# Performance work log

Hardware: AMD Instinct MI355X
Metric: run time of the kernel (lower is better)

Reference implementation:

```python
import jax, jax.numpy as jnp
import numpy as np

B, S, H = 48, 512, 768
E, L, P = 128, 16, 256
NER, NREL, NTYPE = 11, 9, 5


def _forward(sequence_output, W_ner1, b_ner1, W_ner2, b_ner2, type_emb,
             W_g1, a_src1, a_dst1, b_g1, g1_gamma, g1_beta,
             W_g2, a_src2, a_dst2, b_g2, g2_gamma, g2_beta,
             rel_emb, W_r1, b_r1, W_r2, b_r2,
             span_start, span_len, entity_type, pair_head, pair_tail, pair_rel):
    Bv, Sv, Hv = sequence_output.shape
    Ev = span_start.shape[1]
    Pv = pair_head.shape[1]
    # ---- NER classifier head (Linear-ReLU-Linear; dropout inactive at eval) ----
    ner_logits = jax.nn.relu(sequence_output @ W_ner1 + b_ner1) @ W_ner2 + b_ner2  # [B,S,11]
    # ---- entity span attention pooling ----
    pos = jnp.arange(L)
    idx = span_start[..., None] + pos                              # [B,E,L]
    tok = sequence_output[jnp.arange(Bv)[:, None, None], idx]      # [B,E,L,H]
    mask = pos[None, None, :] <= span_len[..., None]               # span covers start..start+len inclusive
    cnt = mask.sum(-1)[..., None].astype(sequence_output.dtype)
    mean = (tok * mask[..., None]).sum(2) / cnt                    # [B,E,H]
    scores = jnp.einsum('belh,beh->bel', tok, mean)
    w = jax.nn.softmax(jnp.where(mask, scores, -jnp.inf), axis=-1)
    pooled = jnp.einsum('bel,belh->beh', w, tok)
    x = pooled + jax.lax.stop_gradient(type_emb[entity_type])      # type emb added under no_grad
    # ---- kNN graph (cosine sim, k=5 -> top 6, threshold 0.1, self loops; built under no_grad) ----
    xs = jax.lax.stop_gradient(x)
    xn = xs / jnp.maximum(jnp.linalg.norm(xs, axis=-1, keepdims=True), 1e-12)
    sim = jnp.einsum('bih,bjh->bij', xn, xn)                       # [B,E,E]
    vals, nbr = jax.lax.top_k(sim, 6)                              # k+1 neighbours incl. self
    valid = (vals > 0.1) & (nbr != jnp.arange(Ev)[None, :, None])
    A = (jax.nn.one_hot(nbr, Ev) * valid[..., None]).sum(2) > 0   # A[b, src, tgt]
    A = A | jnp.eye(Ev, dtype=bool)[None]

    def gat(h_in, W, a_s, a_d, bias, heads, fdim, concat):
        h = (h_in @ W).reshape(Bv, Ev, heads, fdim)
        s = jnp.einsum('behf,hf->beh', h, a_s)
        d = jnp.einsum('behf,hf->beh', h, a_d)
        e = jax.nn.leaky_relu(s[:, :, None, :] + d[:, None, :, :], 0.2)  # [B,src,tgt,heads]
        alpha = jax.nn.softmax(jnp.where(A[..., None], e, -jnp.inf), axis=1)  # softmax over sources per target
        out = jnp.einsum('bsth,bshf->bthf', alpha, h)
        out = out.reshape(Bv, Ev, heads * fdim) if concat else out.mean(2)
        return out + bias

    def ln(v, g, b):
        m = v.mean(-1, keepdims=True)
        var = ((v - m) ** 2).mean(-1, keepdims=True)
        return (v - m) / jnp.sqrt(var + 1e-5) * g + b

    g1 = jax.nn.elu(ln(gat(x, W_g1, a_src1, a_dst1, b_g1, 4, 128, True), g1_gamma, g1_beta))
    ent = jax.nn.elu(ln(gat(g1, W_g2, a_src2, a_dst2, b_g2, 1, 64, False), g2_gamma, g2_beta))  # [B,E,64]
    # ---- relation classifier over candidate pairs ----
    bi = jnp.arange(Bv)[:, None]
    head = ent[bi, pair_head]                                      # [B,P,64]
    tail = ent[bi, pair_tail]
    cls = jnp.broadcast_to(sequence_output[:, None, 0, :], (Bv, Pv, Hv))
    feat = jnp.concatenate([head, tail, rel_emb[pair_rel], cls], axis=-1)  # [B,P,928]
    rel_logits = (jax.nn.relu(feat @ W_r1 + b_r1) @ W_r2 + b_r2)[..., 0]   # [B,P]
    return ner_logits, rel_logits


def setup_inputs() -> dict:
    key = jax.random.key(0)
    ks = jax.random.split(key, 24)
    f = lambda k, sh: jax.random.normal(k, sh, jnp.float32)
    p = lambda k, sh: f(k, sh) * 0.02
    return {
        'sequence_output': f(ks[0], (B, S, H)),
        'span_start': jax.random.randint(ks[1], (B, E), 0, S - L),
        'span_len': jax.random.randint(ks[2], (B, E), 0, L),
        'entity_type': jax.random.randint(ks[3], (B, E), 0, NTYPE),
        'pair_head': jax.random.randint(ks[4], (B, P), 0, E),
        'pair_tail': jax.random.randint(ks[5], (B, P), 0, E),
        'pair_rel': jax.random.randint(ks[6], (B, P), 0, NREL),
        'W_ner1': p(ks[7], (H, 256)), 'b_ner1': jnp.zeros((256,), jnp.float32),
        'W_ner2': p(ks[8], (256, NER)), 'b_ner2': jnp.zeros((NER,), jnp.float32),
        'type_emb': p(ks[9], (NTYPE, H)),
        'W_g1': p(ks[10], (H, 512)), 'a_src1': p(ks[11], (4, 128)), 'a_dst1': p(ks[12], (4, 128)),
        'b_g1': jnp.zeros((512,), jnp.float32),
        'g1_gamma': jnp.ones((512,), jnp.float32), 'g1_beta': jnp.zeros((512,), jnp.float32),
        'W_g2': p(ks[13], (512, 64)), 'a_src2': p(ks[14], (1, 64)), 'a_dst2': p(ks[15], (1, 64)),
        'b_g2': jnp.zeros((64,), jnp.float32),
        'g2_gamma': jnp.ones((64,), jnp.float32), 'g2_beta': jnp.zeros((64,), jnp.float32),
        'rel_emb': p(ks[16], (NREL, 32)),
        'W_r1': p(ks[17], (64 * 2 + 32 + H, 256)), 'b_r1': jnp.zeros((256,), jnp.float32),
        'W_r2': p(ks[18], (256, 1)), 'b_r2': jnp.zeros((1,), jnp.float32),
    }


def reference(sequence_output, span_start, span_len, entity_type, pair_head, pair_tail, pair_rel,
              W_ner1, b_ner1, W_ner2, b_ner2, type_emb,
              W_g1, a_src1, a_dst1, b_g1, g1_gamma, g1_beta,
              W_g2, a_src2, a_dst2, b_g2, g2_gamma, g2_beta,
              rel_emb, W_r1, b_r1, W_r2, b_r2):
    return _forward(sequence_output, W_ner1, b_ner1, W_ner2, b_ner2, type_emb,
                    W_g1, a_src1, a_dst1, b_g1, g1_gamma, g1_beta,
                    W_g2, a_src2, a_dst2, b_g2, g2_gamma, g2_beta,
                    rel_emb, W_r1, b_r1, W_r2, b_r2,
                    span_start, span_len, entity_type, pair_head, pair_tail, pair_rel)
```

## Files before the change

### kernel.cpp

```cpp
#include <hip/hip_runtime.h>
#include <hip/hip_bf16.h>
#include <math.h>

#define Bq 48
#define Sq 512
#define Hq 768
#define Eq 128
#define Lq 16
#define Pq 256
#define NERq 11
#define NER_TOT (Bq*Sq*NERq)

typedef __attribute__((ext_vector_type(8))) short s16x8;
typedef __attribute__((ext_vector_type(4))) float f32x4;
#define MFMA16(a,b,c) __builtin_amdgcn_mfma_f32_16x16x32_bf16(a,b,c,0,0,0)

__device__ __forceinline__ unsigned short f2bf(float f){
  union{float f; unsigned u;} v; v.f=f;
  unsigned r = v.u + 0x7fffu + ((v.u>>16)&1u);
  return (unsigned short)(r>>16);
}
__device__ __forceinline__ float bfu2f(unsigned short h){
  union{unsigned u; float f;} c; c.u = ((unsigned)h)<<16; return c.f;
}

__global__ __launch_bounds__(256) void k_prep(const float* __restrict__ W1, const float* __restrict__ W2,
      const float* __restrict__ Wg1, const float* __restrict__ Wr1,
      unsigned short* __restrict__ W1t, unsigned short* __restrict__ W2t,
      unsigned short* __restrict__ Wg1t, unsigned short* __restrict__ Wr1t){
  int i = blockIdx.x*256 + threadIdx.x;
  if (i < 196608){
    int n = i/768, k = i - n*768;
    W1t[i] = f2bf(W1[k*256 + n]);
  } else if (i < 200704){
    int j = i - 196608; int n = j>>8, k = j&255;
    W2t[j] = (n < NERq) ? f2bf(W2[k*NERq + n]) : 0;
  } else if (i < 593920){
    int j = i - 200704; int n = j/768, k = j - n*768;
    Wg1t[j] = f2bf(Wg1[k*512 + n]);
  } else {
    int j = i - 593920; int n = j/928, k = j - n*928;
    Wr1t[j] = f2bf(Wr1[k*256 + n]);
  }
}

__global__ __launch_bounds__(256) void k_ner(const float* __restrict__ seq, const unsigned short* __restrict__ W1t,
      const float* __restrict__ b1, const unsigned short* __restrict__ W2t, const float* __restrict__ b2,
      float* __restrict__ out){
  __shared__ unsigned short As[32*776];
  unsigned short* Hs = As;
  int tid = threadIdx.x;
  size_t row0 = (size_t)blockIdx.x*32;
  const float4* src = (const float4*)(seq + row0*Hq);
  for (int v=tid; v<6144; v+=256){
    float4 f = src[v];
    int r = v/192, k = (v - r*192)*4;
    ushort4 h = { f2bf(f.x), f2bf(f.y), f2bf(f.z), f2bf(f.w) };
    *(ushort4*)&As[r*776 + k] = h;
  }
  __syncthreads();
  int wave = tid>>6, lane = tid&63, m_ = lane&15, kq = lane>>4;
  int n0 = wave*64;
  const f32x4 z = {0.f,0.f,0.f,0.f};
  f32x4 acc[2][4];
  #pragma unroll
  for (int rt=0;rt<2;rt++)
    #pragma unroll
    for (int ct=0;ct<4;ct++) acc[rt][ct]=z;
  const unsigned short* Wb = W1t + (size_t)(n0 + m_)*768 + kq*8;
  for (int k0=0; k0<768; k0+=32){
    s16x8 a0 = *(const s16x8*)&As[m_*776 + k0 + kq*8];
    s16x8 a1 = *(const s16x8*)&As[(16+m_)*776 + k0 + kq*8];
    s16x8 b0 = *(const s16x8*)(Wb + k0);
    s16x8 b1v = *(const s16x8*)(Wb + 16*768 + k0);
    s16x8 b2v = *(const s16x8*)(Wb + 32*768 + k0);
    s16x8 b3v = *(const s16x8*)(Wb + 48*768 + k0);
    acc[0][0]=MFMA16(a0,b0 ,acc[0][0]); acc[1][0]=MFMA16(a1,b0 ,acc[1][0]);
    acc[0][1]=MFMA16(a0,b1v,acc[0][1]); acc[1][1]=MFMA16(a1,b1v,acc[1][1]);
    acc[0][2]=MFMA16(a0,b2v,acc[0][2]); acc[1][2]=MFMA16(a1,b2v,acc[1][2]);
    acc[0][3]=MFMA16(a0,b3v,acc[0][3]); acc[1][3]=MFMA16(a1,b3v,acc[1][3]);
  }
  __syncthreads();
  #pragma unroll
  for (int ct=0;ct<4;ct++){
    int col = n0 + ct*16 + m_;
    float bb = b1[col];
    #pragma unroll
    for (int rt=0;rt<2;rt++)
      #pragma unroll
      for (int rg=0;rg<4;rg++){
        int row = rt*16 + kq*4 + rg;
        Hs[row*264 + col] = f2bf(fmaxf(acc[rt][ct][rg] + bb, 0.f));
      }
  }
  __syncthreads();
  if (wave < 2){
    f32x4 a2 = z;
    for (int k0=0; k0<256; k0+=32){
      s16x8 a = *(const s16x8*)&Hs[(wave*16 + m_)*264 + k0 + kq*8];
      s16x8 b = *(const s16x8*)&W2t[m_*256 + k0 + kq*8];
      a2 = MFMA16(a,b,a2);
    }
    if (m_ < NERq){
      float bb = b2[m_];
      #pragma unroll
      for (int rg=0;rg<4;rg++){
        int row = wave*16 + kq*4 + rg;
        out[(row0+row)*NERq + m_] = a2[rg] + bb;
      }
    }
  }
}

__global__ __launch_bounds__(256) void k_span(const float* __restrict__ seq, const int* __restrict__ sstart,
      const int* __restrict__ slen, const int* __restrict__ etype, const float* __restrict__ type_emb,
      float* __restrict__ x, float* __restrict__ inv){
  __shared__ float red16[4][16];
  __shared__ float wv[16];
  __shared__ float redn[4];
  int be = blockIdx.x;
  int b = be >> 7;
  int tid = threadIdx.x;
  int wave = tid>>6, lane = tid&63;
  int st = sstart[be], ln = slen[be];
  int cnt = ln + 1;
  const float* base = seq + ((size_t)b*Sq + st)*Hq;
  float tokr[16][3];
  #pragma unroll
  for (int l=0;l<16;l++){
    if (l < cnt){
      tokr[l][0] = base[l*768 + tid];
      tokr[l][1] = base[l*768 + tid + 256];
      tokr[l][2] = base[l*768 + tid + 512];
    } else {
      tokr[l][0]=0.f; tokr[l][1]=0.f; tokr[l][2]=0.f;
    }
  }
  float meanr[3];
  #pragma unroll
  for (int c=0;c<3;c++){
    float s=0.f;
    #pragma unroll
    for (int l=0;l<16;l++) if (l < cnt) s += tokr[l][c];
    meanr[c] = s/(float)cnt;
  }
  #pragma unroll
  for (int l=0;l<16;l++){
    if (l < cnt){
      float p = tokr[l][0]*meanr[0] + tokr[l][1]*meanr[1] + tokr[l][2]*meanr[2];
      #pragma unroll
      for (int off=32; off; off>>=1) p += __shfl_down(p, off, 64);
      if (lane==0) red16[wave][l] = p;
    }
  }
  __syncthreads();
  if (tid==0){
    float sc[16];
    for (int l=0;l<cnt;l++) sc[l] = red16[0][l]+red16[1][l]+red16[2][l]+red16[3][l];
    float m=-1e30f;
    for (int l=0;l<cnt;l++) m = fmaxf(m, sc[l]);
    float ssum=0.f;
    float e[16];
    for (int l=0;l<16;l++){
      e[l] = (l<cnt) ? expf(sc[l]-m) : 0.f;
      ssum += e[l];
    }
    float rs = 1.f/ssum;
    for (int l=0;l<16;l++) wv[l] = e[l]*rs;
  }
  __syncthreads();
  const float* te = type_emb + (size_t)etype[be]*Hq;
  float nrm = 0.f;
  #pragma unroll
  for (int c=0;c<3;c++){
    int h = tid + c*256;
    float p=0.f;
    #pragma unroll
    for (int l=0;l<16;l++) if (l < cnt) p += wv[l]*tokr[l][c];
    float xv = p + te[h];
    x[(size_t)be*Hq + h] = xv;
    nrm += xv*xv;
  }
  #pragma unroll
  for (int off=32; off; off>>=1) nrm += __shfl_down(nrm, off, 64);
  if (lane==0) redn[wave]=nrm;
  __syncthreads();
  if (tid==0){
    float t = redn[0]+redn[1]+redn[2]+redn[3];
    inv[be] = 1.f/fmaxf(sqrtf(t), 1e-12f);
  }
}

__global__ __launch_bounds__(256) void k_sim(const float* __restrict__ x, const float* __restrict__ inv,
                                             float* __restrict__ sim){
  __shared__ float As[128][33];
  __shared__ float Bs[128][33];
  int b = blockIdx.z;
  int i0 = blockIdx.y*32, j0 = blockIdx.x*32;
  int tid = threadIdx.x;
  int ty = tid>>4, tx = tid&15;
  float acc[2][2] = {{0.f,0.f},{0.f,0.f}};
  const float* xb = x + (size_t)b*Eq*Hq;
  for (int k0=0;k0<768;k0+=128){
    for (int idx=tid; idx<1024; idx+=256){
      int kq = idx&31, r = idx>>5;
      float4 va = *(const float4*)&xb[(size_t)(i0+r)*768 + k0 + kq*4];
      float4 vb = *(const float4*)&xb[(size_t)(j0+r)*768 + k0 + kq*4];
      As[kq*4+0][r]=va.x; As[kq*4+1][r]=va.y; As[kq*4+2][r]=va.z; As[kq*4+3][r]=va.w;
      Bs[kq*4+0][r]=vb.x; Bs[kq*4+1][r]=vb.y; Bs[kq*4+2][r]=vb.z; Bs[kq*4+3][r]=vb.w;
    }
    __syncthreads();
    for (int kk=0;kk<128;kk++){
      float a0=As[kk][ty*2], a1=As[kk][ty*2+1];
      float b0=Bs[kk][tx*2], b1=Bs[kk][tx*2+1];
      acc[0][0]=fmaf(a0,b0,acc[0][0]); acc[0][1]=fmaf(a0,b1,acc[0][1]);
      acc[1][0]=fmaf(a1,b0,acc[1][0]); acc[1][1]=fmaf(a1,b1,acc[1][1]);
    }
    __syncthreads();
  }
  float invi[2], invj[2];
  invi[0]=inv[b*Eq + i0+ty*2]; invi[1]=inv[b*Eq + i0+ty*2+1];
  invj[0]=inv[b*Eq + j0+tx*2]; invj[1]=inv[b*Eq + j0+tx*2+1];
  float* sb = sim + (size_t)b*Eq*Eq;
  #pragma unroll
  for (int r=0;r<2;r++)
    #pragma unroll
    for (int c=0;c<2;c++)
      sb[(size_t)(i0+ty*2+r)*Eq + j0+tx*2+c] = acc[r][c]*invi[r]*invj[c];
}

__global__ __launch_bounds__(256) void k_topk(const float* __restrict__ sim, unsigned char* __restrict__ A){
  int row = blockIdx.x*4 + (threadIdx.x>>6);
  int lane = threadIdx.x & 63;
  int b = row>>7, i = row&127;
  const float* r = sim + (size_t)b*Eq*Eq + (size_t)i*Eq;
  float x0 = r[lane], x1 = r[64+lane];
  unsigned char a0=0, a1=0;
  #pragma unroll
  for (int k=0;k<6;k++){
    float m; int idx;
    if (x0 >= x1){ m=x0; idx=lane; } else { m=x1; idx=64+lane; }
    #pragma unroll
    for (int off=32; off; off>>=1){
      float om = __shfl_xor(m, off, 64);
      int oi = __shfl_xor(idx, off, 64);
      if (om > m || (om == m && oi < idx)){ m = om; idx = oi; }
    }
    if (m > 0.1f && idx != i){
      if (idx == lane) a0 = 1;
      if (idx == 64+lane) a1 = 1;
    }
    if (idx == lane) x0 = -1e30f;
    if (idx == 64+lane) x1 = -1e30f;
  }
  if (lane == i) a0 = 1;
  if (64+lane == i) a1 = 1;
  unsigned char* Ar = A + (size_t)b*Eq*Eq + (size_t)i*Eq;
  Ar[lane] = a0; Ar[64+lane] = a1;
}

__global__ __launch_bounds__(256) void k_h1(const float* __restrict__ x, const unsigned short* __restrict__ Wg1t,
                                            float* __restrict__ h1){
  __shared__ unsigned short As[32*776];
  int tid = threadIdx.x;
  size_t row0 = (size_t)blockIdx.x*32;
  int nb = blockIdx.y*256;
  const float4* src = (const float4*)(x + row0*Hq);
  for (int v=tid; v<6144; v+=256){
    float4 f = src[v];
    int r = v/192, k = (v - r*192)*4;
    ushort4 h = { f2bf(f.x), f2bf(f.y), f2bf(f.z), f2bf(f.w) };
    *(ushort4*)&As[r*776 + k] = h;
  }
  __syncthreads();
  int wave = tid>>6, lane = tid&63, m_ = lane&15, kq = lane>>4;
  int n0 = wave*64;
  const f32x4 z = {0.f,0.f,0.f,0.f};
  f32x4 acc[2][4];
  #pragma unroll
  for (int rt=0;rt<2;rt++)
    #pragma unroll
    for (int ct=0;ct<4;ct++) acc[rt][ct]=z;
  const unsigned short* Wb = Wg1t + (size_t)(nb + n0 + m_)*768 + kq*8;
  for (int k0=0; k0<768; k0+=32){
    s16x8 a0 = *(const s16x8*)&As[m_*776 + k0 + kq*8];
    s16x8 a1 = *(const s16x8*)&As[(16+m_)*776 + k0 + kq*8];
    s16x8 b0 = *(const s16x8*)(Wb + k0);
    s16x8 b1v = *(const s16x8*)(Wb + 16*768 + k0);
    s16x8 b2v = *(const s16x8*)(Wb + 32*768 + k0);
    s16x8 b3v = *(const s16x8*)(Wb + 48*768 + k0);
    acc[0][0]=MFMA16(a0,b0 ,acc[0][0]); acc[1][0]=MFMA16(a1,b0 ,acc[1][0]);
    acc[0][1]=MFMA16(a0,b1v,acc[0][1]); acc[1][1]=MFMA16(a1,b1v,acc[1][1]);
    acc[0][2]=MFMA16(a0,b2v,acc[0][2]); acc[1][2]=MFMA16(a1,b2v,acc[1][2]);
    acc[0][3]=MFMA16(a0,b3v,acc[0][3]); acc[1][3]=MFMA16(a1,b3v,acc[1][3]);
  }
  #pragma unroll
  for (int ct=0;ct<4;ct++){
    int col = nb + n0 + ct*16 + m_;
    #pragma unroll
    for (int rt=0;rt<2;rt++)
      #pragma unroll
      for (int rg=0;rg<4;rg++){
        int row = rt*16 + kq*4 + rg;
        h1[(row0+row)*512 + col] = acc[rt][ct][rg];
      }
  }
}

__global__ __launch_bounds__(256) void k_sd1(const float* __restrict__ h1, const float* __restrict__ as1,
      const float* __restrict__ ad1, float* __restrict__ s1, float* __restrict__ d1){
  int gw = (blockIdx.x*256 + threadIdx.x)>>6;
  int lane = threadIdx.x & 63;
  if (gw >= Bq*Eq) return;
  const float* hr = h1 + (size_t)gw*512;
  int hd = lane>>4;
  int i0 = lane*8;
  float4 va = *(const float4*)&hr[i0];
  float4 vb = *(const float4*)&hr[i0+4];
  float av[8] = {va.x,va.y,va.z,va.w,vb.x,vb.y,vb.z,vb.w};
  float ps=0.f, pd=0.f;
  #pragma unroll
  for (int u=0;u<8;u++){
    ps += av[u]*as1[i0+u];
    pd += av[u]*ad1[i0+u];
  }
  #pragma unroll
  for (int off=8; off; off>>=1){ ps += __shfl_down(ps,off,16); pd += __shfl_down(pd,off,16); }
  if ((lane&15)==0){ s1[(size_t)gw*4+hd]=ps; d1[(size_t)gw*4+hd]=pd; }
}

__global__ __launch_bounds__(256) void k_gat1(const float* __restrict__ h1, const float* __restrict__ s1,
      const float* __restrict__ d1, const unsigned char* __restrict__ A,
      const float* __restrict__ bg1, const float* __restrict__ gam, const float* __restrict__ bet,
      float* __restrict__ g1){
  __shared__ float alpha[4][128];
  __shared__ int nbr[128];
  __shared__ int nnz_s;
  __shared__ float outv[512];
  __shared__ float red[8];
  __shared__ float mv_s, rstd_s;
  int bt = blockIdx.x; int b = bt>>7, t = bt&127;
  int tid = threadIdx.x;
  if (tid==0) nnz_s = 0;
  __syncthreads();
  const unsigned char* Ab = A + (size_t)b*Eq*Eq;
  if (tid < 128){
    if (Ab[(size_t)tid*Eq + t]){ int p = atomicAdd(&nnz_s, 1); nbr[p] = tid; }
  }
  __syncthreads();
  int nnz = nnz_s;
  for (int idx=tid; idx<nnz*4; idx+=256){
    int k = idx>>2, hd = idx&3;
    int s = nbr[k];
    float ev = s1[(size_t)(b*Eq+s)*4 + hd] + d1[(size_t)bt*4 + hd];
    alpha[hd][k] = ev>0.f ? ev : 0.2f*ev;
  }
  __syncthreads();
  if (tid < 4){
    float m = -1e30f;
    for (int k=0;k<nnz;k++) m = fmaxf(m, alpha[tid][k]);
    float ss = 0.f;
    for (int k=0;k<nnz;k++){ float e = expf(alpha[tid][k]-m); alpha[tid][k]=e; ss+=e; }
    float rs = 1.f/ss;
    for (int k=0;k<nnz;k++) alpha[tid][k] *= rs;
  }
  __syncthreads();
  for (int c=tid; c<512; c+=256){
    int hd = c>>7;
    float o = 0.f;
    for (int k=0;k<nnz;k++) o += alpha[hd][k] * h1[((size_t)b*Eq + nbr[k])*512 + c];
    outv[c] = o + bg1[c];
  }
  __syncthreads();
  float ls=0.f, lq=0.f;
  for (int c=tid;c<512;c+=256){ float v=outv[c]; ls+=v; lq+=v*v; }
  #pragma unroll
  for (int off=32; off; off>>=1){ ls += __shfl_down(ls,off,64); lq += __shfl_down(lq,off,64); }
  int wv_ = tid>>6;
  if ((tid&63)==0){ red[wv_]=ls; red[4+wv_]=lq; }
  __syncthreads();
  if (tid==0){
    float sm=red[0]+red[1]+red[2]+red[3], sq=red[4]+red[5]+red[6]+red[7];
    float m = sm/512.f; mv_s = m; rstd_s = rsqrtf(sq/512.f - m*m + 1e-5f);
  }
  __syncthreads();
  for (int c=tid;c<512;c+=256){
    float v = (outv[c]-mv_s)*rstd_s*gam[c] + bet[c];
    g1[(size_t)bt*512 + c] = v>0.f ? v : expm1f(v);
  }
}

__global__ __launch_bounds__(256) void k_h2(const float* __restrict__ g1, const float* __restrict__ Wg2,
      const float* __restrict__ as2, const float* __restrict__ ad2,
      float* __restrict__ h2, float* __restrict__ s2, float* __restrict__ d2){
  __shared__ float gt[16*512];
  int tid=threadIdx.x;
  size_t row0 = (size_t)blockIdx.x*16;
  const float4* src = (const float4*)(g1 + row0*512);
  for (int v=tid; v<2048; v+=256) *(float4*)&gt[v*4] = src[v];
  __syncthreads();
  int w = tid>>6, lane = tid&63;
  float acc[4];
  #pragma unroll
  for (int r=0;r<4;r++) acc[r]=0.f;
  for (int k=0;k<512;k+=4){
    float w0=Wg2[(k+0)*64+lane];
    float w1=Wg2[(k+1)*64+lane];
    float w2=Wg2[(k+2)*64+lane];
    float w3=Wg2[(k+3)*64+lane];
    #pragma unroll
    for (int r=0;r<4;r++){
      const float4 t = *(const float4*)&gt[(w*4+r)*512 + k];
      acc[r]=fmaf(t.x,w0,acc[r]);
      acc[r]=fmaf(t.y,w1,acc[r]);
      acc[r]=fmaf(t.z,w2,acc[r]);
      acc[r]=fmaf(t.w,w3,acc[r]);
    }
  }
  float as_=as2[lane], ad_=ad2[lane];
  #pragma unroll
  for (int r=0;r<4;r++){
    size_t row = row0 + w*4 + r;
    h2[row*64 + lane] = acc[r];
    float ps = acc[r]*as_, pd = acc[r]*ad_;
    #pragma unroll
    for (int off=32; off; off>>=1){ ps += __shfl_down(ps,off,64); pd += __shfl_down(pd,off,64); }
    if (lane==0){ s2[row]=ps; d2[row]=pd; }
  }
}

__global__ __launch_bounds__(64) void k_gat2(const float* __restrict__ h2, const float* __restrict__ s2,
      const float* __restrict__ d2, const unsigned char* __restrict__ A,
      const float* __restrict__ bg2, const float* __restrict__ gam, const float* __restrict__ bet,
      float* __restrict__ ent){
  __shared__ float alpha[128];
  __shared__ int nbr[128];
  __shared__ int nnz_s;
  int bt = blockIdx.x; int b = bt>>7, t = bt&127;
  int tid=threadIdx.x;
  if (tid==0) nnz_s=0;
  __syncthreads();
  const unsigned char* Ab = A + (size_t)b*Eq*Eq;
  for (int s=tid; s<128; s+=64) if (Ab[(size_t)s*Eq + t]) { int p=atomicAdd(&nnz_s,1); nbr[p]=s; }
  __syncthreads();
  int nnz = nnz_s;
  float dt = d2[bt];
  for (int k=tid; k<nnz; k+=64){
    float ev = s2[(size_t)b*Eq + nbr[k]] + dt;
    alpha[k] = ev>0.f ? ev : 0.2f*ev;
  }
  __syncthreads();
  if (tid==0){
    float m=-1e30f;
    for (int k=0;k<nnz;k++) m = fmaxf(m, alpha[k]);
    float ss=0.f;
    for (int k=0;k<nnz;k++){ float e=expf(alpha[k]-m); alpha[k]=e; ss+=e; }
    float rs=1.f/ss;
    for (int k=0;k<nnz;k++) alpha[k]*=rs;
  }
  __syncthreads();
  float o = bg2[tid];
  for (int k=0;k<nnz;k++) o += alpha[k]*h2[((size_t)b*Eq + nbr[k])*64 + tid];
  float sv = o, qv = o*o;
  #pragma unroll
  for (int off=1; off<64; off<<=1){ sv += __shfl_xor(sv,off,64); qv += __shfl_xor(qv,off,64); }
  float m = sv*(1.f/64.f);
  float var = qv*(1.f/64.f) - m*m;
  float v = (o-m)*rsqrtf(var+1e-5f)*gam[tid] + bet[tid];
  ent[(size_t)bt*64 + tid] = v>0.f ? v : expm1f(v);
}

__global__ __launch_bounds__(256) void k_rel(const float* __restrict__ ent, const float* __restrict__ seq,
      const float* __restrict__ rel_emb, const int* __restrict__ ph, const int* __restrict__ pt,
      const int* __restrict__ pr, const unsigned short* __restrict__ Wr1t, const float* __restrict__ br1,
      const float* __restrict__ Wr2, const float* __restrict__ br2, float* __restrict__ out){
  __shared__ unsigned short As[32*936];
  unsigned short* Hs = As;
  int tid = threadIdx.x;
  int p0 = blockIdx.x*32;
  for (int idx=tid; idx<32*928; idx+=256){
    int r = idx/928, c = idx - r*928;
    int gp = p0 + r; int b = gp>>8, pp = gp&255;
    float v;
    if (c < 64)      v = ent[((size_t)b*Eq + ph[b*Pq+pp])*64 + c];
    else if (c<128)  v = ent[((size_t)b*Eq + pt[b*Pq+pp])*64 + (c-64)];
    else if (c<160)  v = rel_emb[pr[b*Pq+pp]*32 + (c-128)];
    else             v = seq[(size_t)b*Sq*Hq + (c-160)];
    As[r*936 + c] = f2bf(v);
  }
  __syncthreads();
  int wave = tid>>6, lane = tid&63, m_ = lane&15, kq = lane>>4;
  int n0 = wave*64;
  const f32x4 z = {0.f,0.f,0.f,0.f};
  f32x4 acc[2][4];
  #pragma unroll
  for (int rt=0;rt<2;rt++)
    #pragma unroll
    for (int ct=0;ct<4;ct++) acc[rt][ct]=z;
  const unsigned short* Wb = Wr1t + (size_t)(n0 + m_)*928 + kq*8;
  for (int k0=0; k0<928; k0+=32){
    s16x8 a0 = *(const s16x8*)&As[m_*936 + k0 + kq*8];
    s16x8 a1 = *(const s16x8*)&As[(16+m_)*936 + k0 + kq*8];
    s16x8 b0 = *(const s16x8*)(Wb + k0);
    s16x8 b1v = *(const s16x8*)(Wb + 16*928 + k0);
    s16x8 b2v = *(const s16x8*)(Wb + 32*928 + k0);
    s16x8 b3v = *(const s16x8*)(Wb + 48*928 + k0);
    acc[0][0]=MFMA16(a0,b0 ,acc[0][0]); acc[1][0]=MFMA16(a1,b0 ,acc[1][0]);
    acc[0][1]=MFMA16(a0,b1v,acc[0][1]); acc[1][1]=MFMA16(a1,b1v,acc[1][1]);
    acc[0][2]=MFMA16(a0,b2v,acc[0][2]); acc[1][2]=MFMA16(a1,b2v,acc[1][2]);
    acc[0][3]=MFMA16(a0,b3v,acc[0][3]); acc[1][3]=MFMA16(a1,b3v,acc[1][3]);
  }
  __syncthreads();
  #pragma unroll
  for (int ct=0;ct<4;ct++){
    int col = n0 + ct*16 + m_;
    float bb = br1[col];
    #pragma unroll
    for (int rt=0;rt<2;rt++)
      #pragma unroll
      for (int rg=0;rg<4;rg++){
        int row = rt*16 + kq*4 + rg;
        Hs[row*264 + col] = f2bf(fmaxf(acc[rt][ct][rg] + bb, 0.f));
      }
  }
  __syncthreads();
  {
    int r2 = tid>>3, q = tid&7;
    float p = 0.f;
    for (int u=q*32; u<q*32+32; u++) p += bfu2f(Hs[r2*264+u]) * Wr2[u];
    #pragma unroll
    for (int off=4; off; off>>=1) p += __shfl_down(p, off, 8);
    if (q==0) out[NER_TOT + p0 + r2] = p + br2[0];
  }
}

extern "C" void kernel_launch(void* const* d_in, const int* in_sizes, int n_in,
                              void* d_out, int out_size, void* d_ws, size_t ws_size,
                              hipStream_t stream){
  const float* seq      = (const float*)d_in[0];
  const int*  sstart   = (const int*)d_in[1];
  const int*  slen     = (const int*)d_in[2];
  const int*  etype    = (const int*)d_in[3];
  const int*  ph       = (const int*)d_in[4];
  const int*  pt       = (const int*)d_in[5];
  const int*  pr       = (const int*)d_in[6];
  const float* W_ner1   = (const float*)d_in[7];
  const float* b_ner1   = (const float*)d_in[8];
  const float* W_ner2   = (const float*)d_in[9];
  const float* b_ner2   = (const float*)d_in[10];
  const float* type_emb = (const float*)d_in[11];
  const float* W_g1     = (const float*)d_in[12];
  const float* a_src1   = (const float*)d_in[13];
  const float* a_dst1   = (const float*)d_in[14];
  const float* b_g1     = (const float*)d_in[15];
  const float* g1_gamma = (const float*)d_in[16];
  const float* g1_beta  = (const float*)d_in[17];
  const float* W_g2     = (const float*)d_in[18];
  const float* a_src2   = (const float*)d_in[19];
  const float* a_dst2   = (const float*)d_in[20];
  const float* b_g2     = (const float*)d_in[21];
  const float* g2_gamma = (const float*)d_in[22];
  const float* g2_beta  = (const float*)d_in[23];
  const float* rel_emb  = (const float*)d_in[24];
  const float* W_r1     = (const float*)d_in[25];
  const float* b_r1     = (const float*)d_in[26];
  const float* W_r2     = (const float*)d_in[27];
  const float* b_r2     = (const float*)d_in[28];
  float* outp = (float*)d_out;

  float* x    = (float*)d_ws;
  float* g1   = x;
  float* inv  = x   + (size_t)Bq*Eq*Hq;
  float* sim  = inv + Bq*Eq;
  float* h2   = sim;
  float* s2   = h2  + (size_t)Bq*Eq*64;
  float* d2   = s2  + Bq*Eq;
  float* h1   = sim + (size_t)Bq*Eq*Eq;
  float* s1   = h1  + (size_t)Bq*Eq*512;
  float* d1   = s1  + Bq*Eq*4;
  float* entp = d1  + Bq*Eq*4;
  unsigned char* A = (unsigned char*)(entp + (size_t)Bq*Eq*64);
  unsigned short* W1t  = (unsigned short*)(A + (size_t)Bq*Eq*Eq);
  unsigned short* W2t  = W1t  + 196608;
  unsigned short* Wg1t = W2t  + 4096;
  unsigned short* Wr1t = Wg1t + 393216;

  k_prep<<<3248, 256, 0, stream>>>(W_ner1, W_ner2, W_g1, W_r1, W1t, W2t, Wg1t, Wr1t);
  k_ner <<<768, 256, 0, stream>>>(seq, W1t, b_ner1, W2t, b_ner2, outp);
  k_span<<<Bq*Eq, 256, 0, stream>>>(seq, sstart, slen, etype, type_emb, x, inv);
  k_sim <<<dim3(4,4,Bq), 256, 0, stream>>>(x, inv, sim);
  k_topk<<<1536, 256, 0, stream>>>(sim, A);
  k_h1  <<<dim3(192,2), 256, 0, stream>>>(x, Wg1t, h1);
  k_sd1 <<<1536, 256, 0, stream>>>(h1, a_src1, a_dst1, s1, d1);
  k_gat1<<<Bq*Eq, 256, 0, stream>>>(h1, s1, d1, A, b_g1, g1_gamma, g1_beta, g1);
  k_h2  <<<384, 256, 0, stream>>>(g1, W_g2, a_src2, a_dst2, h2, s2, d2);
  k_gat2<<<Bq*Eq, 64, 0, stream>>>(h2, s2, d2, A, b_g2, g2_gamma, g2_beta, entp);
  k_rel <<<384, 256, 0, stream>>>(entp, seq, rel_emb, ph, pt, pr, Wr1t, b_r1, W_r2, b_r2, outp);
}
```

Measured before the change: 447.9 us.

## Split GEMM kernels into single-wave blocks reading activations directly from global

The NER head is split into two kernels, with the hidden layer written to a bf16 workspace. The first-layer GEMM and the GAT h1 GEMM now run as 64-thread blocks that load fp32 activations straight from global memory and convert them to bf16 in registers, instead of staging them through LDS. The relation kernel halves its row tile to 16 pairs per block, which doubles the grid. The goal is more blocks, more occupancy and no LDS staging or syncs. The cost is that each activation row is now re-read from global or L2 by every output-column block, plus an extra launch and a hidden-layer round trip for NER.

Result: slower. 466.9 us (+4.2%).

```diff
diff --git a/kernel.cpp b/kernel.cpp
--- a/kernel.cpp
+++ b/kernel.cpp
@@ -22,6 +22,12 @@
 }
 __device__ __forceinline__ float bfu2f(unsigned short h){
   union{unsigned u; float f;} c; c.u = ((unsigned)h)<<16; return c.f;
+}
+__device__ __forceinline__ s16x8 pack_bf8(float4 lo, float4 hi){
+  union { s16x8 v; unsigned short u[8]; } r;
+  r.u[0]=f2bf(lo.x); r.u[1]=f2bf(lo.y); r.u[2]=f2bf(lo.z); r.u[3]=f2bf(lo.w);
+  r.u[4]=f2bf(hi.x); r.u[5]=f2bf(hi.y); r.u[6]=f2bf(hi.z); r.u[7]=f2bf(hi.w);
+  return r.v;
 }
 
 __global__ __launch_bounds__(256) void k_prep(const float* __restrict__ W1, const float* __restrict__ W2,
@@ -44,43 +50,36 @@
   }
 }
 
-__global__ __launch_bounds__(256) void k_ner(const float* __restrict__ seq, const unsigned short* __restrict__ W1t,
-      const float* __restrict__ b1, const unsigned short* __restrict__ W2t, const float* __restrict__ b2,
-      float* __restrict__ out){
-  __shared__ unsigned short As[32*776];
-  unsigned short* Hs = As;
-  int tid = threadIdx.x;
+__global__ __launch_bounds__(64) void k_ner1(const float* __restrict__ seq, const unsigned short* __restrict__ W1t,
+      const float* __restrict__ b1, unsigned short* __restrict__ hid){
+  int lane = threadIdx.x, m_ = lane&15, kq = lane>>4;
   size_t row0 = (size_t)blockIdx.x*32;
-  const float4* src = (const float4*)(seq + row0*Hq);
-  for (int v=tid; v<6144; v+=256){
-    float4 f = src[v];
-    int r = v/192, k = (v - r*192)*4;
-    ushort4 h = { f2bf(f.x), f2bf(f.y), f2bf(f.z), f2bf(f.w) };
-    *(ushort4*)&As[r*776 + k] = h;
-  }
-  __syncthreads();
-  int wave = tid>>6, lane = tid&63, m_ = lane&15, kq = lane>>4;
-  int n0 = wave*64;
+  int n0 = blockIdx.y*64;
+  const float* A0 = seq + (row0 + m_)*Hq + kq*8;
+  const float* A1 = A0 + 16*Hq;
+  const unsigned short* Wb = W1t + (size_t)(n0 + m_)*768 + kq*8;
   const f32x4 z = {0.f,0.f,0.f,0.f};
   f32x4 acc[2][4];
   #pragma unroll
   for (int rt=0;rt<2;rt++)
     #pragma unroll
     for (int ct=0;ct<4;ct++) acc[rt][ct]=z;
-  const unsigned short* Wb = W1t + (size_t)(n0 + m_)*768 + kq*8;
   for (int k0=0; k0<768; k0+=32){
-    s16x8 a0 = *(const s16x8*)&As[m_*776 + k0 + kq*8];
-    s16x8 a1 = *(const s16x8*)&As[(16+m_)*776 + k0 + kq*8];
+    float4 l0 = *(const float4*)(A0 + k0);
+    float4 h0 = *(const float4*)(A0 + k0 + 4);
+    float4 l1 = *(const float4*)(A1 + k0);
+    float4 h1v = *(const float4*)(A1 + k0 + 4);
     s16x8 b0 = *(const s16x8*)(Wb + k0);
     s16x8 b1v = *(const s16x8*)(Wb + 16*768 + k0);
     s16x8 b2v = *(const s16x8*)(Wb + 32*768 + k0);
     s16x8 b3v = *(const s16x8*)(Wb + 48*768 + k0);
+    s16x8 a0 = pack_bf8(l0,h0);
+    s16x8 a1 = pack_bf8(l1,h1v);
     acc[0][0]=MFMA16(a0,b0 ,acc[0][0]); acc[1][0]=MFMA16(a1,b0 ,acc[1][0]);
     acc[0][1]=MFMA16(a0,b1v,acc[0][1]); acc[1][1]=MFMA16(a1,b1v,acc[1][1]);
     acc[0][2]=MFMA16(a0,b2v,acc[0][2]); acc[1][2]=MFMA16(a1,b2v,acc[1][2]);
     acc[0][3]=MFMA16(a0,b3v,acc[0][3]); acc[1][3]=MFMA16(a1,b3v,acc[1][3]);
   }
-  __syncthreads();
   #pragma unroll
   for (int ct=0;ct<4;ct++){
     int col = n0 + ct*16 + m_;
@@ -90,25 +89,26 @@
       #pragma unroll
       for (int rg=0;rg<4;rg++){
         int row = rt*16 + kq*4 + rg;
-        Hs[row*264 + col] = f2bf(fmaxf(acc[rt][ct][rg] + bb, 0.f));
+        hid[(row0+row)*256 + col] = f2bf(fmaxf(acc[rt][ct][rg] + bb, 0.f));
       }
   }
-  __syncthreads();
-  if (wave < 2){
-    f32x4 a2 = z;
-    for (int k0=0; k0<256; k0+=32){
-      s16x8 a = *(const s16x8*)&Hs[(wave*16 + m_)*264 + k0 + kq*8];
-      s16x8 b = *(const s16x8*)&W2t[m_*256 + k0 + kq*8];
-      a2 = MFMA16(a,b,a2);
-    }
-    if (m_ < NERq){
-      float bb = b2[m_];
-      #pragma unroll
-      for (int rg=0;rg<4;rg++){
-        int row = wave*16 + kq*4 + rg;
-        out[(row0+row)*NERq + m_] = a2[rg] + bb;
-      }
-    }
+}
+
+__global__ __launch_bounds__(64) void k_ner2(const unsigned short* __restrict__ hid,
+      const unsigned short* __restrict__ W2t, const float* __restrict__ b2, float* __restrict__ out){
+  int lane = threadIdx.x, m_ = lane&15, kq = lane>>4;
+  size_t row0 = (size_t)blockIdx.x*16;
+  f32x4 a2 = {0.f,0.f,0.f,0.f};
+  for (int k0=0;k0<256;k0+=32){
+    s16x8 a = *(const s16x8*)&hid[(row0+m_)*256 + k0 + kq*8];
+    s16x8 b = *(const s16x8*)&W2t[m_*256 + k0 + kq*8];
+    a2 = MFMA16(a,b,a2);
+  }
+  if (m_ < NERq){
+    float bb = b2[m_];
+    #pragma unroll
+    for (int rg=0;rg<4;rg++)
+      out[(row0+kq*4+rg)*NERq + m_] = a2[rg] + bb;
   }
 }
 
@@ -259,36 +259,31 @@
   Ar[lane] = a0; Ar[64+lane] = a1;
 }
 
-__global__ __launch_bounds__(256) void k_h1(const float* __restrict__ x, const unsigned short* __restrict__ Wg1t,
-                                            float* __restrict__ h1){
-  __shared__ unsigned short As[32*776];
-  int tid = threadIdx.x;
+__global__ __launch_bounds__(64) void k_h1(const float* __restrict__ x, const unsigned short* __restrict__ Wg1t,
+                                           float* __restrict__ h1){
+  int lane = threadIdx.x, m_ = lane&15, kq = lane>>4;
   size_t row0 = (size_t)blockIdx.x*32;
-  int nb = blockIdx.y*256;
-  const float4* src = (const float4*)(x + row0*Hq);
-  for (int v=tid; v<6144; v+=256){
-    float4 f = src[v];
-    int r = v/192, k = (v - r*192)*4;
-    ushort4 h = { f2bf(f.x), f2bf(f.y), f2bf(f.z), f2bf(f.w) };
-    *(ushort4*)&As[r*776 + k] = h;
-  }
-  __syncthreads();
-  int wave = tid>>6, lane = tid&63, m_ = lane&15, kq = lane>>4;
-  int n0 = wave*64;
+  int n0 = blockIdx.y*64;
+  const float* A0 = x + (row0 + m_)*Hq + kq*8;
+  const float* A1 = A0 + 16*Hq;
+  const unsigned short* Wb = Wg1t + (size_t)(n0 + m_)*768 + kq*8;
   const f32x4 z = {0.f,0.f,0.f,0.f};
   f32x4 acc[2][4];
   #pragma unroll
   for (int rt=0;rt<2;rt++)
     #pragma unroll
     for (int ct=0;ct<4;ct++) acc[rt][ct]=z;
-  const unsigned short* Wb = Wg1t + (size_t)(nb + n0 + m_)*768 + kq*8;
   for (int k0=0; k0<768; k0+=32){
-    s16x8 a0 = *(const s16x8*)&As[m_*776 + k0 + kq*8];
-    s16x8 a1 = *(const s16x8*)&As[(16+m_)*776 + k0 + kq*8];
+    float4 l0 = *(const float4*)(A0 + k0);
+    float4 h0 = *(const float4*)(A0 + k0 + 4);
+    float4 l1 = *(const float4*)(A1 + k0);
+    float4 h1v = *(const float4*)(A1 + k0 + 4);
     s16x8 b0 = *(const s16x8*)(Wb + k0);
     s16x8 b1v = *(const s16x8*)(Wb + 16*768 + k0);
     s16x8 b2v = *(const s16x8*)(Wb + 32*768 + k0);
     s16x8 b3v = *(const s16x8*)(Wb + 48*768 + k0);
+    s16x8 a0 = pack_bf8(l0,h0);
+    s16x8 a1 = pack_bf8(l1,h1v);
     acc[0][0]=MFMA16(a0,b0 ,acc[0][0]); acc[1][0]=MFMA16(a1,b0 ,acc[1][0]);
     acc[0][1]=MFMA16(a0,b1v,acc[0][1]); acc[1][1]=MFMA16(a1,b1v,acc[1][1]);
     acc[0][2]=MFMA16(a0,b2v,acc[0][2]); acc[1][2]=MFMA16(a1,b2v,acc[1][2]);
@@ -296,7 +291,7 @@
   }
   #pragma unroll
   for (int ct=0;ct<4;ct++){
-    int col = nb + n0 + ct*16 + m_;
+    int col = n0 + ct*16 + m_;
     #pragma unroll
     for (int rt=0;rt<2;rt++)
       #pragma unroll
@@ -474,11 +469,11 @@
       const float* __restrict__ rel_emb, const int* __restrict__ ph, const int* __restrict__ pt,
       const int* __restrict__ pr, const unsigned short* __restrict__ Wr1t, const float* __restrict__ br1,
       const float* __restrict__ Wr2, const float* __restrict__ br2, float* __restrict__ out){
-  __shared__ unsigned short As[32*936];
+  __shared__ unsigned short As[16*936];
   unsigned short* Hs = As;
   int tid = threadIdx.x;
-  int p0 = blockIdx.x*32;
-  for (int idx=tid; idx<32*928; idx+=256){
+  int p0 = blockIdx.x*16;
+  for (int idx=tid; idx<16*928; idx+=256){
     int r = idx/928, c = idx - r*928;
     int gp = p0 + r; int b = gp>>8, pp = gp&255;
     float v;
@@ -492,23 +487,20 @@
   int wave = tid>>6, lane = tid&63, m_ = lane&15, kq = lane>>4;
   int n0 = wave*64;
   const f32x4 z = {0.f,0.f,0.f,0.f};
-  f32x4 acc[2][4];
-  #pragma unroll
-  for (int rt=0;rt<2;rt++)
-    #pragma unroll
-    for (int ct=0;ct<4;ct++) acc[rt][ct]=z;
+  f32x4 acc[4];
+  #pragma unroll
+  for (int ct=0;ct<4;ct++) acc[ct]=z;
   const unsigned short* Wb = Wr1t + (size_t)(n0 + m_)*928 + kq*8;
   for (int k0=0; k0<928; k0+=32){
     s16x8 a0 = *(const s16x8*)&As[m_*936 + k0 + kq*8];
-    s16x8 a1 = *(const s16x8*)&As[(16+m_)*936 + k0 + kq*8];
     s16x8 b0 = *(const s16x8*)(Wb + k0);
     s16x8 b1v = *(const s16x8*)(Wb + 16*928 + k0);
     s16x8 b2v = *(const s16x8*)(Wb + 32*928 + k0);
     s16x8 b3v = *(const s16x8*)(Wb + 48*928 + k0);
-    acc[0][0]=MFMA16(a0,b0 ,acc[0][0]); acc[1][0]=MFMA16(a1,b0 ,acc[1][0]);
-    acc[0][1]=MFMA16(a0,b1v,acc[0][1]); acc[1][1]=MFMA16(a1,b1v,acc[1][1]);
-    acc[0][2]=MFMA16(a0,b2v,acc[0][2]); acc[1][2]=MFMA16(a1,b2v,acc[1][2]);
-    acc[0][3]=MFMA16(a0,b3v,acc[0][3]); acc[1][3]=MFMA16(a1,b3v,acc[1][3]);
+    acc[0]=MFMA16(a0,b0 ,acc[0]);
+    acc[1]=MFMA16(a0,b1v,acc[1]);
+    acc[2]=MFMA16(a0,b2v,acc[2]);
+    acc[3]=MFMA16(a0,b3v,acc[3]);
   }
   __syncthreads();
   #pragma unroll
@@ -516,20 +508,18 @@
     int col = n0 + ct*16 + m_;
     float bb = br1[col];
     #pragma unroll
-    for (int rt=0;rt<2;rt++)
-      #pragma unroll
-      for (int rg=0;rg<4;rg++){
-        int row = rt*16 + kq*4 + rg;
-        Hs[row*264 + col] = f2bf(fmaxf(acc[rt][ct][rg] + bb, 0.f));
-      }
+    for (int rg=0;rg<4;rg++){
+      int row = kq*4 + rg;
+      Hs[row*264 + col] = f2bf(fmaxf(acc[ct][rg] + bb, 0.f));
+    }
   }
   __syncthreads();
   {
-    int r2 = tid>>3, q = tid&7;
+    int r2 = tid>>4, q = tid&15;
     float p = 0.f;
-    for (int u=q*32; u<q*32+32; u++) p += bfu2f(Hs[r2*264+u]) * Wr2[u];
-    #pragma unroll
-    for (int off=4; off; off>>=1) p += __shfl_down(p, off, 8);
+    for (int u=q*16; u<q*16+16; u++) p += bfu2f(Hs[r2*264+u]) * Wr2[u];
+    #pragma unroll
+    for (int off=8; off; off>>=1) p += __shfl_down(p, off, 16);
     if (q==0) out[NER_TOT + p0 + r2] = p + br2[0];
   }
 }
@@ -584,16 +574,18 @@
   unsigned short* W2t  = W1t  + 196608;
   unsigned short* Wg1t = W2t  + 4096;
   unsigned short* Wr1t = Wg1t + 393216;
+  unsigned short* hid  = (unsigned short*)sim;
 
   k_prep<<<3248, 256, 0, stream>>>(W_ner1, W_ner2, W_g1, W_r1, W1t, W2t, Wg1t, Wr1t);
-  k_ner <<<768, 256, 0, stream>>>(seq, W1t, b_ner1, W2t, b_ner2, outp);
+  k_ner1<<<dim3(768,4), 64, 0, stream>>>(seq, W1t, b_ner1, hid);
+  k_ner2<<<1536, 64, 0, stream>>>(hid, W2t, b_ner2, outp);
   k_span<<<Bq*Eq, 256, 0, stream>>>(seq, sstart, slen, etype, type_emb, x, inv);
   k_sim <<<dim3(4,4,Bq), 256, 0, stream>>>(x, inv, sim);
   k_topk<<<1536, 256, 0, stream>>>(sim, A);
-  k_h1  <<<dim3(192,2), 256, 0, stream>>>(x, Wg1t, h1);
+  k_h1  <<<dim3(192,8), 64, 0, stream>>>(x, Wg1t, h1);
   k_sd1 <<<1536, 256, 0, stream>>>(h1, a_src1, a_dst1, s1, d1);
   k_gat1<<<Bq*Eq, 256, 0, stream>>>(h1, s1, d1, A, b_g1, g1_gamma, g1_beta, g1);
   k_h2  <<<384, 256, 0, stream>>>(g1, W_g2, a_src2, a_dst2, h2, s2, d2);
   k_gat2<<<Bq*Eq, 64, 0, stream>>>(h2, s2, d2, A, b_g2, g2_gamma, g2_beta, entp);
-  k_rel <<<384, 256, 0, stream>>>(entp, seq, rel_emb, ph, pt, pr, Wr1t, b_r1, W_r2, b_r2, outp);
-}
+  k_rel <<<768, 256, 0, stream>>>(entp, seq, rel_emb, ph, pt, pr, Wr1t, b_r1, W_r2, b_r2, outp);
+}
```
